# Performance work log

Measured on AMD Instinct MI355X. Metric: run time of the kernel, lower is better.

Reference implementation:

```python
import jax, jax.numpy as jnp
import numpy as np

EPS_NORM = 1e-12   # torch F.normalize eps
EPS_BN = 1e-5      # BatchNorm1d eps
NEG_SLOPE = 0.01   # LeakyReLU default


def _l2_normalize(x, axis):
    # torch F.normalize: x / max(||x||, eps)
    n = jnp.sqrt(jnp.sum(x * x, axis=axis, keepdims=True))
    return x / jnp.maximum(n, EPS_NORM)


def setup_inputs() -> dict:
    key = jax.random.key(0)
    k1, k2, k3, k4, k5, k6, k7 = jax.random.split(key, 7)
    B, C, N, M, OUT = 8, 128, 4096, 4096, 128
    return {
        "input": jax.random.normal(k1, (B, C, N), dtype=jnp.float32),
        "target_g": jax.random.normal(k2, (B, C, M), dtype=jnp.float32),
        "weight": jax.random.normal(k3, (C, OUT), dtype=jnp.float32) * (1.0 / np.sqrt(OUT)),
        "gamma": jax.random.normal(k4, (OUT,), dtype=jnp.float32),
        "beta": jax.random.normal(k5, (OUT,), dtype=jnp.float32),
        "running_mean": jax.random.normal(k6, (OUT,), dtype=jnp.float32),
        "running_var": jax.random.uniform(k7, (OUT,), dtype=jnp.float32, minval=0.5, maxval=1.5),
    }


def reference(input, target_g, weight, gamma, beta, running_mean, running_var):
    # input: [B, C, N], target_g: [B, C, M]
    # cosine-similarity adjacency: [B, M, N]
    tg = _l2_normalize(target_g, axis=1)
    inp_n = _l2_normalize(input, axis=1)
    adj = jnp.einsum('bcm,bcn->bmn', tg, inp_n)
    adj = jax.nn.softmax(adj, axis=-1)
    # aggregate: [B, M, C]
    agg = jnp.einsum('bmn,bcn->bmc', adj, input)
    # project: [B, M, OUT] -> permute to [B, OUT, M]
    out = jnp.einsum('bmc,co->bom', agg, weight)
    # LeakyReLU then BatchNorm1d (eval mode, running stats)
    out = jnp.where(out >= 0, out, NEG_SLOPE * out)
    inv = jax.lax.rsqrt(running_var + EPS_BN)
    out = (out - running_mean[None, :, None]) * (inv * gamma)[None, :, None] + beta[None, :, None]
    return out
```

## Files before the change

kernel.cpp:

```cpp
#include <hip/hip_runtime.h>
#include <hip/hip_bf16.h>

#define BATCH 8
#define CDIM 128
#define NDIM 4096

typedef __bf16 bf16x8 __attribute__((ext_vector_type(8)));
typedef float f32x4 __attribute__((ext_vector_type(4)));

#define QT_OFF 0u
#define KT_OFF 8388608u
#define VB_OFF 16777216u
#define WT_OFF 25165824u
#define SC_OFF (WT_OFF + 32768u)
#define BI_OFF (SC_OFF + 512u)

__device__ __forceinline__ f32x4 mfma16(bf16x8 a, bf16x8 b, f32x4 c) {
    return __builtin_amdgcn_mfma_f32_16x16x32_bf16(a, b, c, 0, 0, 0);
}

__device__ __forceinline__ unsigned pack2bf(float a, float b) {
    unsigned short ul = __builtin_bit_cast(unsigned short, (__bf16)a);
    unsigned short uh = __builtin_bit_cast(unsigned short, (__bf16)b);
    return (unsigned)ul | ((unsigned)uh << 16);
}

__device__ __forceinline__ void glds16(const void* g, void* l) {
    __builtin_amdgcn_global_load_lds((__attribute__((address_space(1))) void*)(void*)g,
                                     (__attribute__((address_space(3))) void*)l, 16, 0, 0);
}

__global__ __launch_bounds__(256) void prep_nt(const float* __restrict__ input,
                                               const float* __restrict__ tg,
                                               void* __restrict__ ws) {
    __shared__ float Tt[64][129];
    __shared__ float psum[4][64];
    __shared__ float rn[64];
    const int n0 = blockIdx.x * 64;
    const int b  = blockIdx.y;
    const int tid = threadIdx.x;
    const float* src = (blockIdx.z == 0 ? input : tg) + (size_t)b * CDIM * NDIM;

    #pragma unroll
    for (int i = 0; i < 8; ++i) {
        int f = tid + i * 256;
        int c = f >> 4, j4 = f & 15;
        float4 v = *(const float4*)(src + (size_t)c * NDIM + n0 + j4 * 4);
        Tt[j4 * 4 + 0][c] = v.x;
        Tt[j4 * 4 + 1][c] = v.y;
        Tt[j4 * 4 + 2][c] = v.z;
        Tt[j4 * 4 + 3][c] = v.w;
    }
    __syncthreads();
    {
        int j = tid & 63, part = tid >> 6;
        float ss = 0.f;
        #pragma unroll 8
        for (int c = part * 32; c < part * 32 + 32; ++c) { float x = Tt[j][c]; ss += x * x; }
        psum[part][j] = ss;
    }
    __syncthreads();
    if (tid < 64) {
        float s = psum[0][tid] + psum[1][tid] + psum[2][tid] + psum[3][tid];
        rn[tid] = 1.0f / fmaxf(sqrtf(s), 1e-12f);
    }
    __syncthreads();

    __hip_bfloat16* dstT = (__hip_bfloat16*)((char*)ws + (blockIdx.z == 0 ? KT_OFF : QT_OFF))
                           + ((size_t)b * NDIM + n0) * CDIM;
    #pragma unroll
    for (int i = 0; i < 8; ++i) {
        int f = tid + i * 256;
        int j = f >> 5, c4 = f & 31;
        float r = rn[j];
        float4 v = *(const float4*)&Tt[j][c4 * 4];
        uint2 pk; pk.x = pack2bf(v.x * r, v.y * r); pk.y = pack2bf(v.z * r, v.w * r);
        *(uint2*)((unsigned short*)dstT + (size_t)j * CDIM + c4 * 4) = pk;
    }
    if (blockIdx.z == 0) {
        __hip_bfloat16* vb = (__hip_bfloat16*)((char*)ws + VB_OFF) + (size_t)b * CDIM * NDIM + n0;
        #pragma unroll
        for (int i = 0; i < 8; ++i) {
            int f = tid + i * 256;
            int c = f >> 4, j4 = f & 15;
            float x0 = Tt[j4 * 4 + 0][c], x1 = Tt[j4 * 4 + 1][c];
            float x2 = Tt[j4 * 4 + 2][c], x3 = Tt[j4 * 4 + 3][c];
            uint2 pv; pv.x = pack2bf(x0, x1); pv.y = pack2bf(x2, x3);
            *(uint2*)((unsigned short*)vb + (size_t)c * NDIM + j4 * 4) = pv;
        }
    }
}

__global__ __launch_bounds__(256) void prep_w(const float* __restrict__ wgt,
                                              const float* __restrict__ gamma,
                                              const float* __restrict__ beta,
                                              const float* __restrict__ mean,
                                              const float* __restrict__ var,
                                              void* __restrict__ ws) {
    __hip_bfloat16* wT = (__hip_bfloat16*)((char*)ws + WT_OFF);
    float* sc = (float*)((char*)ws + SC_OFF);
    float* bi = (float*)((char*)ws + BI_OFF);
    const int tid = threadIdx.x;
    #pragma unroll
    for (int i = 0; i < 64; ++i) {
        int f = tid + i * 256;
        int c = f >> 7, o = f & 127;
        wT[o * 128 + c] = __hip_bfloat16(wgt[c * 128 + o]);
    }
    if (tid < 128) {
        float inv = rsqrtf(var[tid] + 1e-5f);
        float s = inv * gamma[tid];
        sc[tid] = s;
        bi[tid] = beta[tid] - mean[tid] * s;
    }
}

__global__ __launch_bounds__(512, 4) void flash3(const void* __restrict__ ws_,
                                                 float* __restrict__ out) {
    extern __shared__ char smem[];
    const char* ws = (const char*)ws_;
    const __hip_bfloat16* Qt = (const __hip_bfloat16*)(ws + QT_OFF);
    const __hip_bfloat16* Kt = (const __hip_bfloat16*)(ws + KT_OFF);
    const __hip_bfloat16* Vb = (const __hip_bfloat16*)(ws + VB_OFF);
    const __hip_bfloat16* wT = (const __hip_bfloat16*)(ws + WT_OFF);
    const float* scale = (const float*)(ws + SC_OFF);
    const float* bias  = (const float*)(ws + BI_OFF);

    const int b  = blockIdx.y;
    const int m0 = blockIdx.x * 64;
    const int tid = threadIdx.x;
    const int w = tid >> 6, lane = tid & 63;
    const int h = w >> 2, wq = w & 3;
    const int li = lane & 15, q = lane >> 4;
    const int ns = wq >> 1, ms = wq & 1;
    const int cs = wq >> 1;

    const __hip_bfloat16* kgb = Kt + (size_t)b * NDIM * CDIM;
    const __hip_bfloat16* vgb = Vb + (size_t)b * CDIM * NDIM;

    bf16x8 qf[2][4];
    #pragma unroll
    for (int mb = 0; mb < 2; ++mb) {
        const __hip_bfloat16* qrow = Qt + ((size_t)b * NDIM + m0 + ms * 32 + mb * 16 + li) * CDIM;
        #pragma unroll
        for (int ks = 0; ks < 4; ++ks)
            qf[mb][ks] = *(const bf16x8*)(qrow + ks * 32 + q * 8);
    }

    unsigned kOff[2][4];
    #pragma unroll
    for (int nb = 0; nb < 2; ++nb)
        #pragma unroll
        for (int ks = 0; ks < 4; ++ks) {
            int n = ns * 32 + nb * 16 + li;
            kOff[nb][ks] = h * 32768 + n * 256 + (((ks * 4 + q) ^ li)) * 16;
        }
    unsigned vOff[2][4];
    #pragma unroll
    for (int k2 = 0; k2 < 2; ++k2)
        #pragma unroll
        for (int ca = 0; ca < 4; ++ca) {
            int c = cs * 64 + ca * 16 + li;
            vOff[k2][ca] = h * 32768 + 16384 + c * 128 + (((k2 * 4 + q) ^ (li & 7))) * 16;
        }
    unsigned pOff[2][2];
    #pragma unroll
    for (int k2 = 0; k2 < 2; ++k2)
        #pragma unroll
        for (int mb = 0; mb < 2; ++mb)
            pOff[k2][mb] = 65536 + h * 8192 + (ms * 32 + mb * 16 + li) * 128
                           + (((k2 * 8 + q * 2) ^ ((li & 7) << 1))) * 8;
    unsigned wOff[2][2];
    #pragma unroll
    for (int nb = 0; nb < 2; ++nb)
        #pragma unroll
        for (int mb = 0; mb < 2; ++mb)
            wOff[nb][mb] = 65536 + h * 8192 + (ms * 32 + mb * 16 + li) * 128
                           + (((ns * 8 + nb * 4 + q) ^ ((li & 7) << 1))) * 8;

    const __hip_bfloat16* gK[4]; const __hip_bfloat16* gV[4];
    unsigned lKo[4], lVo[4];
    #pragma unroll
    for (int i = 0; i < 4; ++i) {
        int s = (wq * 4 + i) * 64 + lane;
        int n = s >> 4, sl = s & 15;
        int cc = sl ^ (n & 15);
        gK[i] = kgb + (size_t)(h * 2048 + n) * CDIM + cc * 8;
        lKo[i] = h * 32768 + (wq * 4 + i) * 1024;
        int c = s >> 3, sl8 = s & 7;
        int nc = sl8 ^ (c & 7);
        gV[i] = vgb + (size_t)c * NDIM + h * 2048 + nc * 8;
        lVo[i] = h * 32768 + 16384 + (wq * 4 + i) * 1024;
    }

    const f32x4 z4 = {0.f, 0.f, 0.f, 0.f};
    f32x4 oacc[4][2];
    #pragma unroll
    for (int ca = 0; ca < 4; ++ca) { oacc[ca][0] = z4; oacc[ca][1] = z4; }
    float lac0 = 0.f, lac1 = 0.f;

    for (int it = 0; it < 32; ++it) {
        __syncthreads();
        #pragma unroll
        for (int i = 0; i < 4; ++i) { glds16(gK[i], smem + lKo[i]); gK[i] += 64 * CDIM; }
        #pragma unroll
        for (int i = 0; i < 4; ++i) { glds16(gV[i], smem + lVo[i]); gV[i] += 64; }
        __syncthreads();

        #pragma unroll
        for (int nb = 0; nb < 2; ++nb) {
            f32x4 st0 = z4, st1 = z4;
            #pragma unroll
            for (int ks = 0; ks < 4; ++ks) {
                bf16x8 kf = *(const bf16x8*)(smem + kOff[nb][ks]);
                st0 = mfma16(kf, qf[0][ks], st0);
                st1 = mfma16(kf, qf[1][ks], st1);
            }
            {
                float p0 = __expf(st0[0] - 1.0f), p1 = __expf(st0[1] - 1.0f);
                float p2 = __expf(st0[2] - 1.0f), p3 = __expf(st0[3] - 1.0f);
                lac0 += (p0 + p1) + (p2 + p3);
                uint2 pk; pk.x = pack2bf(p0, p1); pk.y = pack2bf(p2, p3);
                *(uint2*)(smem + wOff[nb][0]) = pk;
            }
            {
                float p0 = __expf(st1[0] - 1.0f), p1 = __expf(st1[1] - 1.0f);
                float p2 = __expf(st1[2] - 1.0f), p3 = __expf(st1[3] - 1.0f);
                lac1 += (p0 + p1) + (p2 + p3);
                uint2 pk; pk.x = pack2bf(p0, p1); pk.y = pack2bf(p2, p3);
                *(uint2*)(smem + wOff[nb][1]) = pk;
            }
        }
        __syncthreads();

        #pragma unroll
        for (int k2 = 0; k2 < 2; ++k2) {
            bf16x8 pf0 = *(const bf16x8*)(smem + pOff[k2][0]);
            bf16x8 pf1 = *(const bf16x8*)(smem + pOff[k2][1]);
            #pragma unroll
            for (int ca = 0; ca < 4; ++ca) {
                bf16x8 vf = *(const bf16x8*)(smem + vOff[k2][ca]);
                oacc[ca][0] = mfma16(vf, pf0, oacc[ca][0]);
                oacc[ca][1] = mfma16(vf, pf1, oacc[ca][1]);
            }
        }
    }

    lac0 += __shfl_xor(lac0, 16, 64); lac0 += __shfl_xor(lac0, 32, 64);
    lac1 += __shfl_xor(lac1, 16, 64); lac1 += __shfl_xor(lac1, 32, 64);

    __syncthreads();
    float* lLds = (float*)(smem + 34304);
    if (q == 0) {
        lLds[(h * 2 + ns) * 64 + ms * 32 + li] = lac0;
        lLds[(h * 2 + ns) * 64 + ms * 32 + 16 + li] = lac1;
    }
    float* sO32 = (float*)smem;
    if (h == 1) {
        #pragma unroll
        for (int ca = 0; ca < 4; ++ca)
            #pragma unroll
            for (int mb = 0; mb < 2; ++mb)
                #pragma unroll
                for (int r = 0; r < 4; ++r)
                    sO32[(cs * 64 + ca * 16 + q * 4 + r) * 66 + ms * 32 + mb * 16 + li] =
                        oacc[ca][mb][r];
    }
    __syncthreads();
    __hip_bfloat16* sAgg = (__hip_bfloat16*)(smem + 36864);
    if (h == 0) {
        float linv[2]; int mm[2];
        #pragma unroll
        for (int mb = 0; mb < 2; ++mb) {
            int m = ms * 32 + mb * 16 + li;
            mm[mb] = m;
            linv[mb] = 1.0f / (lLds[m] + lLds[64 + m] + lLds[128 + m] + lLds[192 + m]);
        }
        #pragma unroll
        for (int ca = 0; ca < 4; ++ca) {
            #pragma unroll
            for (int mb = 0; mb < 2; ++mb) {
                int m = mm[mb];
                float v0 = (oacc[ca][mb][0] + sO32[(cs*64 + ca*16 + q*4 + 0) * 66 + m]) * linv[mb];
                float v1 = (oacc[ca][mb][1] + sO32[(cs*64 + ca*16 + q*4 + 1) * 66 + m]) * linv[mb];
                float v2 = (oacc[ca][mb][2] + sO32[(cs*64 + ca*16 + q*4 + 2) * 66 + m]) * linv[mb];
                float v3 = (oacc[ca][mb][3] + sO32[(cs*64 + ca*16 + q*4 + 3) * 66 + m]) * linv[mb];
                uint2 pk; pk.x = pack2bf(v0, v1); pk.y = pack2bf(v2, v3);
                int c8 = cs * 16 + ca * 4 + q;
                int slot8 = c8 ^ ((li & 7) << 1);
                *(uint2*)((char*)sAgg + m * 256 + slot8 * 8) = pk;
            }
        }
    }
    __syncthreads();

    const int mslice = (w & 3) * 16;
    const int ohalf = (w >> 2) * 64;
    f32x4 racc[4];
    #pragma unroll
    for (int ob = 0; ob < 4; ++ob) racc[ob] = z4;
    #pragma unroll
    for (int ks = 0; ks < 4; ++ks) {
        int slot8 = ((ks * 4 + q) * 2) ^ ((li & 7) << 1);
        bf16x8 af = *(const bf16x8*)((char*)sAgg + (mslice + li) * 256 + slot8 * 8);
        #pragma unroll
        for (int ob = 0; ob < 4; ++ob) {
            bf16x8 wf = *(const bf16x8*)(wT + (size_t)(ohalf + ob * 16 + li) * CDIM + ks * 32 + q * 8);
            racc[ob] = mfma16(af, wf, racc[ob]);
        }
    }

    float* sRes = (float*)smem;
    #pragma unroll
    for (int ob = 0; ob < 4; ++ob) {
        int o = ohalf + ob * 16 + li;
        float sc = scale[o], bi = bias[o];
        #pragma unroll
        for (int r = 0; r < 4; ++r) {
            float v = racc[ob][r];
            v = (v >= 0.0f) ? v : 0.01f * v;
            v = v * sc + bi;
            sRes[o * 68 + mslice + q * 4 + r] = v;
        }
    }
    __syncthreads();

    float* outb = out + (size_t)b * CDIM * NDIM + m0;
    #pragma unroll
    for (int i = 0; i < 4; ++i) {
        int f = tid + i * 512;
        int o = f >> 4, mq = f & 15;
        *(float4*)(outb + (size_t)o * NDIM + mq * 4) = *(const float4*)(sRes + o * 68 + mq * 4);
    }
}

extern "C" void kernel_launch(void* const* d_in, const int* in_sizes, int n_in,
                              void* d_out, int out_size, void* d_ws, size_t ws_size,
                              hipStream_t stream) {
    const float* input  = (const float*)d_in[0];
    const float* tg     = (const float*)d_in[1];
    const float* weight = (const float*)d_in[2];
    const float* gamma  = (const float*)d_in[3];
    const float* beta   = (const float*)d_in[4];
    const float* rmean  = (const float*)d_in[5];
    const float* rvar   = (const float*)d_in[6];
    float* out = (float*)d_out;

    (void)in_sizes; (void)n_in; (void)out_size; (void)ws_size;

    hipFuncSetAttribute(reinterpret_cast<const void*>(flash3),
                        hipFuncAttributeMaxDynamicSharedMemorySize, 81920);

    dim3 gprep(NDIM / 64, BATCH, 2);
    prep_nt<<<gprep, 256, 0, stream>>>(input, tg, d_ws);
    prep_w<<<dim3(1), 256, 0, stream>>>(weight, gamma, beta, rmean, rvar, d_ws);
    dim3 gflash(NDIM / 64, BATCH);
    flash3<<<gflash, 512, 81920, stream>>>(d_ws, out);
}
```

Measured before the change: 199.5 us.

## Double-buffer K/V tiles with async prefetch and drop split-N warp halves

```diff
diff --git a/kernel.cpp b/kernel.cpp
--- a/kernel.cpp
+++ b/kernel.cpp
@@ -115,7 +115,7 @@
     }
 }
 
-__global__ __launch_bounds__(512, 4) void flash3(const void* __restrict__ ws_,
+__global__ __launch_bounds__(512, 4) void flash4(const void* __restrict__ ws_,
                                                  float* __restrict__ out) {
     extern __shared__ char smem[];
     const char* ws = (const char*)ws_;
@@ -126,14 +126,14 @@
     const float* scale = (const float*)(ws + SC_OFF);
     const float* bias  = (const float*)(ws + BI_OFF);
 
-    const int b  = blockIdx.y;
-    const int m0 = blockIdx.x * 64;
+    const int bx = blockIdx.x;
+    const int b  = bx & 7;
+    const int m0 = (bx >> 3) * 64;
     const int tid = threadIdx.x;
     const int w = tid >> 6, lane = tid & 63;
-    const int h = w >> 2, wq = w & 3;
     const int li = lane & 15, q = lane >> 4;
-    const int ns = wq >> 1, ms = wq & 1;
-    const int cs = wq >> 1;
+    const int ns = w & 3, msS = w >> 2;
+    const int cs = w & 3, msP = w >> 2;
 
     const __hip_bfloat16* kgb = Kt + (size_t)b * NDIM * CDIM;
     const __hip_bfloat16* vgb = Vb + (size_t)b * CDIM * NDIM;
@@ -141,152 +141,148 @@
     bf16x8 qf[2][4];
     #pragma unroll
     for (int mb = 0; mb < 2; ++mb) {
-        const __hip_bfloat16* qrow = Qt + ((size_t)b * NDIM + m0 + ms * 32 + mb * 16 + li) * CDIM;
+        const __hip_bfloat16* qrow = Qt + ((size_t)b * NDIM + m0 + msS * 32 + mb * 16 + li) * CDIM;
         #pragma unroll
         for (int ks = 0; ks < 4; ++ks)
             qf[mb][ks] = *(const bf16x8*)(qrow + ks * 32 + q * 8);
     }
 
-    unsigned kOff[2][4];
-    #pragma unroll
-    for (int nb = 0; nb < 2; ++nb)
+    unsigned kOff[4];
+    {
+        int n = ns * 16 + li;
+        #pragma unroll
+        for (int ks = 0; ks < 4; ++ks)
+            kOff[ks] = n * 256 + (((ks * 4 + q) ^ (n & 7)) * 16);
+    }
+    unsigned vOff[2][2];
+    #pragma unroll
+    for (int ca = 0; ca < 2; ++ca) {
+        int c = cs * 32 + ca * 16 + li;
+        #pragma unroll
+        for (int k2 = 0; k2 < 2; ++k2)
+            vOff[ca][k2] = 16384 + c * 128 + (((k2 * 4 + q) ^ (c & 7)) * 16);
+    }
+    unsigned pOff[2][2];
+    #pragma unroll
+    for (int mb = 0; mb < 2; ++mb) {
+        int m = msP * 32 + mb * 16 + li;
+        #pragma unroll
+        for (int k2 = 0; k2 < 2; ++k2)
+            pOff[mb][k2] = 65536 + m * 128 + (((k2 * 4 + q) ^ (m & 7)) * 16);
+    }
+    unsigned pwOff[2];
+    #pragma unroll
+    for (int mb = 0; mb < 2; ++mb) {
+        int m = msS * 32 + mb * 16 + li;
+        pwOff[mb] = 65536 + m * 128 + (((ns * 2 + (q >> 1)) ^ (m & 7)) * 16) + (q & 1) * 8;
+    }
+
+    const char* kSrc[2]; const char* vSrc[2];
+    unsigned kDst[2], vDst[2];
+    #pragma unroll
+    for (int i = 0; i < 2; ++i) {
+        int d = (w * 2 + i) * 64 + lane;
+        int n = d >> 4, sz = d & 15;
+        int s = (sz & 8) | ((sz & 7) ^ (n & 7));
+        kSrc[i] = (const char*)kgb + n * 256 + s * 16;
+        kDst[i] = (w * 2 + i) * 1024;
+        int c = d >> 3, sz8 = d & 7;
+        int s8 = sz8 ^ (c & 7);
+        vSrc[i] = (const char*)vgb + (size_t)c * 8192 + s8 * 16;
+        vDst[i] = 16384 + (w * 2 + i) * 1024;
+    }
+
+    const f32x4 z4 = {0.f, 0.f, 0.f, 0.f};
+    f32x4 oacc[2][2];
+    oacc[0][0] = z4; oacc[0][1] = z4; oacc[1][0] = z4; oacc[1][1] = z4;
+    float lac0 = 0.f, lac1 = 0.f;
+
+    #pragma unroll
+    for (int i = 0; i < 2; ++i) { glds16(kSrc[i], smem + kDst[i]); kSrc[i] += 16384; }
+    #pragma unroll
+    for (int i = 0; i < 2; ++i) { glds16(vSrc[i], smem + vDst[i]); vSrc[i] += 128; }
+
+    auto body = [&](const unsigned bo, const bool do_pref) {
+        asm volatile("s_waitcnt vmcnt(0) lgkmcnt(0)\ns_barrier" ::: "memory");
+
+        f32x4 st0 = z4, st1 = z4;
         #pragma unroll
         for (int ks = 0; ks < 4; ++ks) {
-            int n = ns * 32 + nb * 16 + li;
-            kOff[nb][ks] = h * 32768 + n * 256 + (((ks * 4 + q) ^ li)) * 16;
-        }
-    unsigned vOff[2][4];
-    #pragma unroll
-    for (int k2 = 0; k2 < 2; ++k2)
-        #pragma unroll
-        for (int ca = 0; ca < 4; ++ca) {
-            int c = cs * 64 + ca * 16 + li;
-            vOff[k2][ca] = h * 32768 + 16384 + c * 128 + (((k2 * 4 + q) ^ (li & 7))) * 16;
-        }
-    unsigned pOff[2][2];
-    #pragma unroll
-    for (int k2 = 0; k2 < 2; ++k2)
-        #pragma unroll
-        for (int mb = 0; mb < 2; ++mb)
-            pOff[k2][mb] = 65536 + h * 8192 + (ms * 32 + mb * 16 + li) * 128
-                           + (((k2 * 8 + q * 2) ^ ((li & 7) << 1))) * 8;
-    unsigned wOff[2][2];
-    #pragma unroll
-    for (int nb = 0; nb < 2; ++nb)
-        #pragma unroll
-        for (int mb = 0; mb < 2; ++mb)
-            wOff[nb][mb] = 65536 + h * 8192 + (ms * 32 + mb * 16 + li) * 128
-                           + (((ns * 8 + nb * 4 + q) ^ ((li & 7) << 1))) * 8;
-
-    const __hip_bfloat16* gK[4]; const __hip_bfloat16* gV[4];
-    unsigned lKo[4], lVo[4];
-    #pragma unroll
-    for (int i = 0; i < 4; ++i) {
-        int s = (wq * 4 + i) * 64 + lane;
-        int n = s >> 4, sl = s & 15;
-        int cc = sl ^ (n & 15);
-        gK[i] = kgb + (size_t)(h * 2048 + n) * CDIM + cc * 8;
-        lKo[i] = h * 32768 + (wq * 4 + i) * 1024;
-        int c = s >> 3, sl8 = s & 7;
-        int nc = sl8 ^ (c & 7);
-        gV[i] = vgb + (size_t)c * NDIM + h * 2048 + nc * 8;
-        lVo[i] = h * 32768 + 16384 + (wq * 4 + i) * 1024;
-    }
-
-    const f32x4 z4 = {0.f, 0.f, 0.f, 0.f};
-    f32x4 oacc[4][2];
-    #pragma unroll
-    for (int ca = 0; ca < 4; ++ca) { oacc[ca][0] = z4; oacc[ca][1] = z4; }
-    float lac0 = 0.f, lac1 = 0.f;
-
-    for (int it = 0; it < 32; ++it) {
-        __syncthreads();
-        #pragma unroll
-        for (int i = 0; i < 4; ++i) { glds16(gK[i], smem + lKo[i]); gK[i] += 64 * CDIM; }
-        #pragma unroll
-        for (int i = 0; i < 4; ++i) { glds16(gV[i], smem + lVo[i]); gV[i] += 64; }
-        __syncthreads();
-
-        #pragma unroll
-        for (int nb = 0; nb < 2; ++nb) {
-            f32x4 st0 = z4, st1 = z4;
+            bf16x8 kf = *(const bf16x8*)(smem + bo + kOff[ks]);
+            st0 = mfma16(kf, qf[0][ks], st0);
+            st1 = mfma16(kf, qf[1][ks], st1);
+        }
+        {
+            float p0 = __expf(st0[0] - 1.0f), p1 = __expf(st0[1] - 1.0f);
+            float p2 = __expf(st0[2] - 1.0f), p3 = __expf(st0[3] - 1.0f);
+            lac0 += (p0 + p1) + (p2 + p3);
+            uint2 pk; pk.x = pack2bf(p0, p1); pk.y = pack2bf(p2, p3);
+            *(uint2*)(smem + pwOff[0]) = pk;
+        }
+        {
+            float p0 = __expf(st1[0] - 1.0f), p1 = __expf(st1[1] - 1.0f);
+            float p2 = __expf(st1[2] - 1.0f), p3 = __expf(st1[3] - 1.0f);
+            lac1 += (p0 + p1) + (p2 + p3);
+            uint2 pk; pk.x = pack2bf(p0, p1); pk.y = pack2bf(p2, p3);
+            *(uint2*)(smem + pwOff[1]) = pk;
+        }
+        if (do_pref) {
+            const unsigned obo = bo ^ 32768u;
             #pragma unroll
-            for (int ks = 0; ks < 4; ++ks) {
-                bf16x8 kf = *(const bf16x8*)(smem + kOff[nb][ks]);
-                st0 = mfma16(kf, qf[0][ks], st0);
-                st1 = mfma16(kf, qf[1][ks], st1);
-            }
-            {
-                float p0 = __expf(st0[0] - 1.0f), p1 = __expf(st0[1] - 1.0f);
-                float p2 = __expf(st0[2] - 1.0f), p3 = __expf(st0[3] - 1.0f);
-                lac0 += (p0 + p1) + (p2 + p3);
-                uint2 pk; pk.x = pack2bf(p0, p1); pk.y = pack2bf(p2, p3);
-                *(uint2*)(smem + wOff[nb][0]) = pk;
-            }
-            {
-                float p0 = __expf(st1[0] - 1.0f), p1 = __expf(st1[1] - 1.0f);
-                float p2 = __expf(st1[2] - 1.0f), p3 = __expf(st1[3] - 1.0f);
-                lac1 += (p0 + p1) + (p2 + p3);
-                uint2 pk; pk.x = pack2bf(p0, p1); pk.y = pack2bf(p2, p3);
-                *(uint2*)(smem + wOff[nb][1]) = pk;
-            }
-        }
-        __syncthreads();
+            for (int i = 0; i < 2; ++i) { glds16(kSrc[i], smem + (obo + kDst[i])); kSrc[i] += 16384; }
+            #pragma unroll
+            for (int i = 0; i < 2; ++i) { glds16(vSrc[i], smem + (obo + vDst[i])); vSrc[i] += 128; }
+        }
+        asm volatile("s_waitcnt lgkmcnt(0)\ns_barrier" ::: "memory");
 
         #pragma unroll
         for (int k2 = 0; k2 < 2; ++k2) {
-            bf16x8 pf0 = *(const bf16x8*)(smem + pOff[k2][0]);
-            bf16x8 pf1 = *(const bf16x8*)(smem + pOff[k2][1]);
-            #pragma unroll
-            for (int ca = 0; ca < 4; ++ca) {
-                bf16x8 vf = *(const bf16x8*)(smem + vOff[k2][ca]);
-                oacc[ca][0] = mfma16(vf, pf0, oacc[ca][0]);
-                oacc[ca][1] = mfma16(vf, pf1, oacc[ca][1]);
-            }
-        }
+            bf16x8 pf0 = *(const bf16x8*)(smem + pOff[0][k2]);
+            bf16x8 pf1 = *(const bf16x8*)(smem + pOff[1][k2]);
+            bf16x8 vf0 = *(const bf16x8*)(smem + bo + vOff[0][k2]);
+            bf16x8 vf1 = *(const bf16x8*)(smem + bo + vOff[1][k2]);
+            oacc[0][0] = mfma16(vf0, pf0, oacc[0][0]);
+            oacc[0][1] = mfma16(vf0, pf1, oacc[0][1]);
+            oacc[1][0] = mfma16(vf1, pf0, oacc[1][0]);
+            oacc[1][1] = mfma16(vf1, pf1, oacc[1][1]);
+        }
+    };
+
+    for (int ii = 0; ii < 32; ++ii) {
+        body(0u, true);
+        body(32768u, ii != 31);
     }
 
     lac0 += __shfl_xor(lac0, 16, 64); lac0 += __shfl_xor(lac0, 32, 64);
     lac1 += __shfl_xor(lac1, 16, 64); lac1 += __shfl_xor(lac1, 32, 64);
 
     __syncthreads();
-    float* lLds = (float*)(smem + 34304);
+    float* lLds = (float*)(smem + 34816);
     if (q == 0) {
-        lLds[(h * 2 + ns) * 64 + ms * 32 + li] = lac0;
-        lLds[(h * 2 + ns) * 64 + ms * 32 + 16 + li] = lac1;
-    }
-    float* sO32 = (float*)smem;
-    if (h == 1) {
-        #pragma unroll
-        for (int ca = 0; ca < 4; ++ca)
-            #pragma unroll
-            for (int mb = 0; mb < 2; ++mb)
-                #pragma unroll
-                for (int r = 0; r < 4; ++r)
-                    sO32[(cs * 64 + ca * 16 + q * 4 + r) * 66 + ms * 32 + mb * 16 + li] =
-                        oacc[ca][mb][r];
+        lLds[ns * 64 + msS * 32 + li] = lac0;
+        lLds[ns * 64 + msS * 32 + 16 + li] = lac1;
     }
     __syncthreads();
     __hip_bfloat16* sAgg = (__hip_bfloat16*)(smem + 36864);
-    if (h == 0) {
+    {
         float linv[2]; int mm[2];
         #pragma unroll
         for (int mb = 0; mb < 2; ++mb) {
-            int m = ms * 32 + mb * 16 + li;
+            int m = msP * 32 + mb * 16 + li;
             mm[mb] = m;
             linv[mb] = 1.0f / (lLds[m] + lLds[64 + m] + lLds[128 + m] + lLds[192 + m]);
         }
         #pragma unroll
-        for (int ca = 0; ca < 4; ++ca) {
+        for (int ca = 0; ca < 2; ++ca) {
             #pragma unroll
             for (int mb = 0; mb < 2; ++mb) {
                 int m = mm[mb];
-                float v0 = (oacc[ca][mb][0] + sO32[(cs*64 + ca*16 + q*4 + 0) * 66 + m]) * linv[mb];
-                float v1 = (oacc[ca][mb][1] + sO32[(cs*64 + ca*16 + q*4 + 1) * 66 + m]) * linv[mb];
-                float v2 = (oacc[ca][mb][2] + sO32[(cs*64 + ca*16 + q*4 + 2) * 66 + m]) * linv[mb];
-                float v3 = (oacc[ca][mb][3] + sO32[(cs*64 + ca*16 + q*4 + 3) * 66 + m]) * linv[mb];
+                float v0 = oacc[ca][mb][0] * linv[mb];
+                float v1 = oacc[ca][mb][1] * linv[mb];
+                float v2 = oacc[ca][mb][2] * linv[mb];
+                float v3 = oacc[ca][mb][3] * linv[mb];
                 uint2 pk; pk.x = pack2bf(v0, v1); pk.y = pack2bf(v2, v3);
-                int c8 = cs * 16 + ca * 4 + q;
+                int c8 = cs * 8 + ca * 4 + q;
                 int slot8 = c8 ^ ((li & 7) << 1);
                 *(uint2*)((char*)sAgg + m * 256 + slot8 * 8) = pk;
             }
@@ -348,12 +344,11 @@
 
     (void)in_sizes; (void)n_in; (void)out_size; (void)ws_size;
 
-    hipFuncSetAttribute(reinterpret_cast<const void*>(flash3),
-                        hipFuncAttributeMaxDynamicSharedMemorySize, 81920);
+    hipFuncSetAttribute(reinterpret_cast<const void*>(flash4),
+                        hipFuncAttributeMaxDynamicSharedMemorySize, 73728);
 
     dim3 gprep(NDIM / 64, BATCH, 2);
     prep_nt<<<gprep, 256, 0, stream>>>(input, tg, d_ws);
     prep_w<<<dim3(1), 256, 0, stream>>>(weight, gamma, beta, rmean, rvar, d_ws);
-    dim3 gflash(NDIM / 64, BATCH);
-    flash3<<<gflash, 512, 81920, stream>>>(d_ws, out);
-}
+    flash4<<<dim3(512), 512, 73728, stream>>>(d_ws, out);
+}
```

After: 200.1 us. Within noise of the previous version (+0.3%).
